# Performance work log

Hardware: AMD Instinct MI355X
Metric: run time of the kernel (lower is better)

## Reference

```python
import jax, jax.numpy as jnp
import numpy as np

B, M, T, N = 128, 256, 512, 512

def setup_inputs() -> dict:
    key = jax.random.key(0)
    ks = jax.random.split(key, 6)
    return {
        "hidden_state": jax.random.normal(ks[0], (B, M), jnp.float32),
        "cell_state": jax.random.normal(ks[1], (B, M), jnp.float32),
        "X": jax.random.normal(ks[2], (B, T, N), jnp.float32),
        "We1": jax.random.normal(ks[3], (2 * M, T), jnp.float32) * 0.05,
        "be1": jnp.zeros((T,), jnp.float32),
        "We2": jax.random.normal(ks[4], (T, T), jnp.float32) * 0.05,
        "be2": jnp.zeros((T,), jnp.float32),
        "v": jax.random.normal(ks[5], (T, 1), jnp.float32) * 0.05,
        "bv": jnp.zeros((1,), jnp.float32),
    }

def reference(hidden_state, cell_state, X, We1, be1, We2, be2, v, bv):
    # concat hidden + cell: [B, 2m]; Dense(T) then broadcast over n (K.repeat)
    hc = jnp.concatenate([hidden_state, cell_state], axis=-1)
    hs = (hc @ We1 + be1)[:, None, :]                 # [B, 1, T] (broadcast over n)
    # Permute X -> [B, n, T], Dense(T): contract over T
    ux = jnp.einsum('btn,tk->bnk', X, We2) + be2      # [B, n, T]
    # add + tanh + Dense(1) fused chain
    e = jnp.tanh(hs + ux) @ v + bv                    # [B, n, 1]
    # Permute -> [B, 1, n], softmax over last axis (n)
    attn = jax.nn.softmax(jnp.swapaxes(e, 1, 2), axis=-1)  # [B, 1, n]
    return attn
```

## Files before the change

### kernel.cpp

```cpp
#include <hip/hip_runtime.h>
#include <hip/hip_bf16.h>


typedef _Float16 half8 __attribute__((ext_vector_type(8)));
typedef _Float16 half2v __attribute__((ext_vector_type(2)));
typedef float floatx4 __attribute__((ext_vector_type(4)));

#define GLOAD_LDS16(gp, lp) __builtin_amdgcn_global_load_lds(                  \
    (const __attribute__((address_space(1))) void*)(const void*)(gp),          \
    (__attribute__((address_space(3))) void*)(void*)(lp), 16, 0, 0)

__device__ __forceinline__ float fast_tanh(float x) {
    float cx = fminf(15.0f, fmaxf(-15.0f, x));
    float e = __expf(2.0f * cx);
    return (e - 1.0f) * __fdividef(1.0f, e + 1.0f);
}

__global__ __launch_bounds__(256) void k_prep_a(const float* __restrict__ We2,
                                                _Float16* __restrict__ Af) {
    __shared__ float w2[32][512];
    const int ts = blockIdx.x;
    for (int idx = threadIdx.x; idx < 32 * 512; idx += 256) {
        int tl = idx >> 9, k = idx & 511;
        w2[tl][k] = We2[(ts * 32 + tl) * 512 + k];
    }
    __syncthreads();
    for (int item = threadIdx.x; item < 32 * 64; item += 256) {
        int c = item >> 6, l = item & 63;
        int k  = c * 16 + (l & 15);
        int tl = (l >> 4) * 8;
        half8 h;
#pragma unroll
        for (int j = 0; j < 8; ++j) h[j] = (_Float16)w2[tl + j][k];
        *(half8*)&Af[(((size_t)ts * 32 + c) * 64 + l) * 8] = h;
    }
}

__global__ __launch_bounds__(256) void k_hs(const float* __restrict__ hidden,
                                            const float* __restrict__ cell,
                                            const float* __restrict__ We1,
                                            const float* __restrict__ be1,
                                            const float* __restrict__ be2,
                                            float* __restrict__ g) {
    __shared__ __align__(16) float hcl[8][512];
    __shared__ float red[4][8][64];
    const int b0 = (blockIdx.x >> 3) << 3;
    const int k0 = (blockIdx.x & 7) << 6;
    for (int idx = threadIdx.x; idx < 8 * 512; idx += 256) {
        int bi = idx >> 9, j = idx & 511;
        hcl[bi][j] = (j < 256) ? hidden[(b0 + bi) * 256 + j]
                               : cell[(b0 + bi) * 256 + j - 256];
    }
    __syncthreads();
    const int kl = threadIdx.x & 63;
    const int jc = threadIdx.x >> 6;
    const int k  = k0 + kl;
    float acc[8] = {};
    for (int j = jc * 128; j < jc * 128 + 128; j += 4) {
        float w0 = We1[(j + 0) * 512 + k];
        float w1 = We1[(j + 1) * 512 + k];
        float w2 = We1[(j + 2) * 512 + k];
        float w3 = We1[(j + 3) * 512 + k];
#pragma unroll
        for (int bi = 0; bi < 8; ++bi) {
            float4 h = *(const float4*)&hcl[bi][j];
            acc[bi] += h.x * w0 + h.y * w1 + h.z * w2 + h.w * w3;
        }
    }
#pragma unroll
    for (int bi = 0; bi < 8; ++bi) red[jc][bi][kl] = acc[bi];
    __syncthreads();
    for (int idx = threadIdx.x; idx < 512; idx += 256) {
        int bi = idx >> 6, kk = idx & 63;
        float s = red[0][bi][kk] + red[1][bi][kk] + red[2][bi][kk] + red[3][bi][kk];
        int kg = k0 + kk;
        g[(b0 + bi) * 512 + kg] = s + be1[kg] + be2[kg];
    }
}

__global__ __launch_bounds__(256, 3) void k_main(const float* __restrict__ X,
                                                 const _Float16* __restrict__ Af,
                                                 const float* __restrict__ g,
                                                 const float* __restrict__ vvec,
                                                 float* __restrict__ Ep) {
    __shared__ __align__(16) float Xs[3][4096];
    const int tid  = threadIdx.x;
    const int lane = tid & 63;
    const int wv   = tid >> 6;
    const int l16  = lane & 15;
    const int lhi  = lane >> 4;
    const int logical = ((blockIdx.x & 7) << 8) | (blockIdx.x >> 3);
    const int kblk = logical & 1;
    const int nt   = (logical >> 1) & 7;
    const int b    = logical >> 4;
    const int n0   = nt << 6;

    const float* Xg = X + (size_t)b * 262144 + n0;
    const _Float16* AgW = Af + (size_t)(kblk * 16 + wv * 4) * 512 + (size_t)lane * 8;

    int xsrc[4], xdst[4];
#pragma unroll
    for (int p = 0; p < 4; ++p) {
        int t_loc = (wv << 4) + (p << 2) + (lane >> 4);
        int c_g   = (lane & 15) ^ (((t_loc >> 3) & 3) << 1);
        xsrc[p] = t_loc * 512 + c_g * 4;
        xdst[p] = ((wv << 4) + (p << 2)) * 64 + lane * 4;
    }
#define XDMA(s_, b_)                                                           \
    { _Pragma("unroll")                                                        \
      for (int p = 0; p < 4; ++p)                                              \
          GLOAD_LDS16(Xg + (size_t)(s_) * 32768 + xsrc[p], &Xs[b_][xdst[p]]); }

    const int q = l16 >> 2, r = l16 & 3;
    int boff[4];
#pragma unroll
    for (int nf = 0; nf < 4; ++nf)
        boff[nf] = lhi * 512 + ((((nf << 2) + q) ^ (lhi << 1)) << 2) + r;

    XDMA(0, 0);
    XDMA(1, 1);

    floatx4 acc[4][4];
#pragma unroll
    for (int a = 0; a < 4; ++a)
#pragma unroll
        for (int c = 0; c < 4; ++c) acc[a][c] = (floatx4){0.f, 0.f, 0.f, 0.f};

#pragma unroll
    for (int s = 0; s < 8; ++s) {
        const int buf = s % 3;
        if (s < 7) asm volatile("s_waitcnt vmcnt(4)" ::: "memory");
        else       asm volatile("s_waitcnt vmcnt(0)" ::: "memory");
        asm volatile("s_waitcnt lgkmcnt(0)" ::: "memory");
        __builtin_amdgcn_sched_barrier(0);
        __builtin_amdgcn_s_barrier();
        __builtin_amdgcn_sched_barrier(0);
        if (s + 2 < 8) XDMA(s + 2, (s + 2) % 3);
#pragma unroll
        for (int ko = 0; ko < 2; ++ko) {
            half8 af[4];
#pragma unroll
            for (int kf = 0; kf < 4; ++kf)
                af[kf] = *(const half8*)
                    (AgW + (size_t)(2 * s + ko) * 16384 + kf * 512);
            half8 bf[4];
#pragma unroll
            for (int nf = 0; nf < 4; ++nf) {
                union { half2v h2[4]; half8 h8; } u;
#pragma unroll
                for (int m = 0; m < 4; ++m) {
                    float f0 = Xs[buf][boff[nf] + ko * 2048 + (2 * m) * 64];
                    float f1 = Xs[buf][boff[nf] + ko * 2048 + (2 * m + 1) * 64];
                    u.h2[m] = __builtin_bit_cast(half2v,
                                  __builtin_amdgcn_cvt_pkrtz(f0, f1));
                }
                bf[nf] = u.h8;
            }
            __builtin_amdgcn_s_setprio(1);
#pragma unroll
            for (int kf = 0; kf < 4; ++kf)
#pragma unroll
                for (int nf = 0; nf < 4; ++nf)
                    acc[kf][nf] = __builtin_amdgcn_mfma_f32_16x16x32_f16(
                        af[kf], bf[nf], acc[kf][nf], 0, 0, 0);
            __builtin_amdgcn_s_setprio(0);
        }
    }
#undef XDMA

    const float* gb = g + b * 512;
    float sacc[4] = {0.f, 0.f, 0.f, 0.f};
#pragma unroll
    for (int kf = 0; kf < 4; ++kf) {
        const int kb = kblk * 256 + wv * 64 + kf * 16 + lhi * 4;
        float g0 = gb[kb + 0], g1 = gb[kb + 1], g2 = gb[kb + 2], g3 = gb[kb + 3];
        float v0 = vvec[kb + 0], v1 = vvec[kb + 1], v2 = vvec[kb + 2], v3 = vvec[kb + 3];
#pragma unroll
        for (int nf = 0; nf < 4; ++nf) {
            sacc[nf] += fast_tanh(acc[kf][nf][0] + g0) * v0;
            sacc[nf] += fast_tanh(acc[kf][nf][1] + g1) * v1;
            sacc[nf] += fast_tanh(acc[kf][nf][2] + g2) * v2;
            sacc[nf] += fast_tanh(acc[kf][nf][3] + g3) * v3;
        }
    }
#pragma unroll
    for (int nf = 0; nf < 4; ++nf) {
        sacc[nf] += __shfl_xor(sacc[nf], 16);
        sacc[nf] += __shfl_xor(sacc[nf], 32);
    }
    __syncthreads();
    float* ered = (float*)&Xs[0][0];
    if (lane < 16) {
#pragma unroll
        for (int nf = 0; nf < 4; ++nf) ered[wv * 64 + nf * 16 + l16] = sacc[nf];
    }
    __syncthreads();
    if (tid < 64) {
        float e = ered[tid] + ered[64 + tid] + ered[128 + tid] + ered[192 + tid];
        Ep[(size_t)kblk * 65536 + b * 512 + n0 + tid] = e;
    }
}

__global__ __launch_bounds__(256) void k_softmax(const float* __restrict__ Ep,
                                                 float* __restrict__ out) {
    __shared__ float rmax[4], rsum[4];
    const int b = blockIdx.x;
    const int tid = threadIdx.x;
    const float* E0 = Ep;
    const float* E1 = Ep + 65536;
    float e0 = E0[b * 512 + tid] + E1[b * 512 + tid];
    float e1 = E0[b * 512 + 256 + tid] + E1[b * 512 + 256 + tid];
    float m = fmaxf(e0, e1);
    for (int o = 32; o > 0; o >>= 1) m = fmaxf(m, __shfl_xor(m, o));
    if ((tid & 63) == 0) rmax[tid >> 6] = m;
    __syncthreads();
    m = fmaxf(fmaxf(rmax[0], rmax[1]), fmaxf(rmax[2], rmax[3]));
    float p0 = __expf(e0 - m), p1 = __expf(e1 - m);
    float ss = p0 + p1;
    for (int o = 32; o > 0; o >>= 1) ss += __shfl_xor(ss, o);
    if ((tid & 63) == 0) rsum[tid >> 6] = ss;
    __syncthreads();
    ss = rsum[0] + rsum[1] + rsum[2] + rsum[3];
    float inv = __fdividef(1.0f, ss);
    out[b * 512 + tid] = p0 * inv;
    out[b * 512 + 256 + tid] = p1 * inv;
}

extern "C" void kernel_launch(void* const* d_in, const int* in_sizes, int n_in,
                              void* d_out, int out_size, void* d_ws, size_t ws_size,
                              hipStream_t stream) {
    const float* hidden = (const float*)d_in[0];
    const float* cell   = (const float*)d_in[1];
    const float* X      = (const float*)d_in[2];
    const float* We1    = (const float*)d_in[3];
    const float* be1    = (const float*)d_in[4];
    const float* We2    = (const float*)d_in[5];
    const float* be2    = (const float*)d_in[6];
    const float* v      = (const float*)d_in[7];
    float* out = (float*)d_out;

    char* ws = (char*)d_ws;
    _Float16* Af = (_Float16*)ws;
    float* g     = (float*)(ws + 524288);
    float* Ep    = (float*)(ws + 786432);

    k_prep_a<<<16, 256, 0, stream>>>(We2, Af);
    k_hs<<<128, 256, 0, stream>>>(hidden, cell, We1, be1, be2, g);
    k_main<<<2048, 256, 0, stream>>>(X, Af, g, v, Ep);
    k_softmax<<<128, 256, 0, stream>>>(Ep, out);
}
```

Before: 83.23 us.

## Stage A fragments in LDS and split warps over k and n

```diff
diff --git a/kernel.cpp b/kernel.cpp
--- a/kernel.cpp
+++ b/kernel.cpp
@@ -78,125 +78,137 @@
     }
 }
 
-__global__ __launch_bounds__(256, 3) void k_main(const float* __restrict__ X,
+__global__ __launch_bounds__(256, 4) void k_main(const float* __restrict__ X,
                                                  const _Float16* __restrict__ Af,
                                                  const float* __restrict__ g,
                                                  const float* __restrict__ vvec,
                                                  float* __restrict__ Ep) {
-    __shared__ __align__(16) float Xs[3][4096];
+    __shared__ __align__(16) _Float16 Ab[8192];
+    __shared__ __align__(16) float    Xs[3][2048];
     const int tid  = threadIdx.x;
     const int lane = tid & 63;
     const int wv   = tid >> 6;
     const int l16  = lane & 15;
     const int lhi  = lane >> 4;
-    const int logical = ((blockIdx.x & 7) << 8) | (blockIdx.x >> 3);
+    const int kw   = wv & 1;
+    const int nw   = wv >> 1;
+    const int logical = (blockIdx.x & 7) * 256 + (blockIdx.x >> 3);
     const int kblk = logical & 1;
     const int nt   = (logical >> 1) & 7;
     const int b    = logical >> 4;
     const int n0   = nt << 6;
 
     const float* Xg = X + (size_t)b * 262144 + n0;
-    const _Float16* AgW = Af + (size_t)(kblk * 16 + wv * 4) * 512 + (size_t)lane * 8;
-
-    int xsrc[4], xdst[4];
-#pragma unroll
-    for (int p = 0; p < 4; ++p) {
-        int t_loc = (wv << 4) + (p << 2) + (lane >> 4);
+    const _Float16* Ag = Af + (size_t)(kblk * 16 + wv * 4) * 512 + (size_t)lane * 8;
+
+    int xsrc[2], xdst[2];
+#pragma unroll
+    for (int p = 0; p < 2; ++p) {
+        int t_loc = wv * 8 + p * 4 + (lane >> 4);
         int c_g   = (lane & 15) ^ (((t_loc >> 3) & 3) << 1);
         xsrc[p] = t_loc * 512 + c_g * 4;
-        xdst[p] = ((wv << 4) + (p << 2)) * 64 + lane * 4;
+        xdst[p] = (wv * 8 + p * 4) * 64 + lane * 4;
     }
 #define XDMA(s_, b_)                                                           \
     { _Pragma("unroll")                                                        \
-      for (int p = 0; p < 4; ++p)                                              \
-          GLOAD_LDS16(Xg + (size_t)(s_) * 32768 + xsrc[p], &Xs[b_][xdst[p]]); }
+      for (int p = 0; p < 2; ++p)                                              \
+          GLOAD_LDS16(Xg + (size_t)(s_) * 16384 + xsrc[p], &Xs[b_][xdst[p]]); }
+#define ADMA(s_)                                                               \
+    { _Pragma("unroll")                                                        \
+      for (int i = 0; i < 4; ++i)                                              \
+          GLOAD_LDS16(Ag + (size_t)(s_) * 16384 + i * 512,                     \
+                      &Ab[(wv * 4 + i) * 512 + lane * 8]); }
 
     const int q = l16 >> 2, r = l16 & 3;
-    int boff[4];
-#pragma unroll
-    for (int nf = 0; nf < 4; ++nf)
-        boff[nf] = lhi * 512 + ((((nf << 2) + q) ^ (lhi << 1)) << 2) + r;
+    int boff[2];
+#pragma unroll
+    for (int nf = 0; nf < 2; ++nf) {
+        int nfe = nw * 2 + nf;
+        boff[nf] = lhi * 512 + ((((nfe << 2) + q) ^ (lhi << 1)) << 2) + r;
+    }
 
     XDMA(0, 0);
+    ADMA(0);
     XDMA(1, 1);
 
-    floatx4 acc[4][4];
-#pragma unroll
-    for (int a = 0; a < 4; ++a)
-#pragma unroll
-        for (int c = 0; c < 4; ++c) acc[a][c] = (floatx4){0.f, 0.f, 0.f, 0.f};
-
-#pragma unroll
-    for (int s = 0; s < 8; ++s) {
+    floatx4 acc[8][2];
+#pragma unroll
+    for (int a = 0; a < 8; ++a) {
+        acc[a][0] = (floatx4){0.f, 0.f, 0.f, 0.f};
+        acc[a][1] = (floatx4){0.f, 0.f, 0.f, 0.f};
+    }
+
+#pragma unroll
+    for (int s = 0; s < 16; ++s) {
         const int buf = s % 3;
-        if (s < 7) asm volatile("s_waitcnt vmcnt(4)" ::: "memory");
-        else       asm volatile("s_waitcnt vmcnt(0)" ::: "memory");
+        if (s < 15) asm volatile("s_waitcnt vmcnt(2)" ::: "memory");
+        else        asm volatile("s_waitcnt vmcnt(0)" ::: "memory");
+        __builtin_amdgcn_sched_barrier(0);
+        __builtin_amdgcn_s_barrier();
+        __builtin_amdgcn_sched_barrier(0);
+        half8 af[8];
+#pragma unroll
+        for (int kf = 0; kf < 8; ++kf)
+            af[kf] = *(const half8*)&Ab[(kw * 8 + kf) * 512 + lane * 8];
+        half8 bf[2];
+#pragma unroll
+        for (int nf = 0; nf < 2; ++nf) {
+            union { half2v h2[4]; half8 h8; } u;
+#pragma unroll
+            for (int m = 0; m < 4; ++m) {
+                float f0 = Xs[buf][boff[nf] + (2 * m) * 64];
+                float f1 = Xs[buf][boff[nf] + (2 * m + 1) * 64];
+                u.h2[m] = __builtin_bit_cast(half2v,
+                              __builtin_amdgcn_cvt_pkrtz(f0, f1));
+            }
+            bf[nf] = u.h8;
+        }
         asm volatile("s_waitcnt lgkmcnt(0)" ::: "memory");
         __builtin_amdgcn_sched_barrier(0);
         __builtin_amdgcn_s_barrier();
         __builtin_amdgcn_sched_barrier(0);
-        if (s + 2 < 8) XDMA(s + 2, (s + 2) % 3);
-#pragma unroll
-        for (int ko = 0; ko < 2; ++ko) {
-            half8 af[4];
-#pragma unroll
-            for (int kf = 0; kf < 4; ++kf)
-                af[kf] = *(const half8*)
-                    (AgW + (size_t)(2 * s + ko) * 16384 + kf * 512);
-            half8 bf[4];
-#pragma unroll
-            for (int nf = 0; nf < 4; ++nf) {
-                union { half2v h2[4]; half8 h8; } u;
-#pragma unroll
-                for (int m = 0; m < 4; ++m) {
-                    float f0 = Xs[buf][boff[nf] + ko * 2048 + (2 * m) * 64];
-                    float f1 = Xs[buf][boff[nf] + ko * 2048 + (2 * m + 1) * 64];
-                    u.h2[m] = __builtin_bit_cast(half2v,
-                                  __builtin_amdgcn_cvt_pkrtz(f0, f1));
-                }
-                bf[nf] = u.h8;
-            }
-            __builtin_amdgcn_s_setprio(1);
-#pragma unroll
-            for (int kf = 0; kf < 4; ++kf)
-#pragma unroll
-                for (int nf = 0; nf < 4; ++nf)
-                    acc[kf][nf] = __builtin_amdgcn_mfma_f32_16x16x32_f16(
-                        af[kf], bf[nf], acc[kf][nf], 0, 0, 0);
-            __builtin_amdgcn_s_setprio(0);
+        if (s < 15) ADMA(s + 1);
+        if (s < 14) XDMA(s + 2, (s + 2) % 3);
+        __builtin_amdgcn_sched_barrier(0);
+        __builtin_amdgcn_s_setprio(1);
+#pragma unroll
+        for (int kf = 0; kf < 8; ++kf) {
+            acc[kf][0] = __builtin_amdgcn_mfma_f32_16x16x32_f16(af[kf], bf[0], acc[kf][0], 0, 0, 0);
+            acc[kf][1] = __builtin_amdgcn_mfma_f32_16x16x32_f16(af[kf], bf[1], acc[kf][1], 0, 0, 0);
         }
+        __builtin_amdgcn_s_setprio(0);
     }
 #undef XDMA
+#undef ADMA
 
     const float* gb = g + b * 512;
-    float sacc[4] = {0.f, 0.f, 0.f, 0.f};
-#pragma unroll
-    for (int kf = 0; kf < 4; ++kf) {
-        const int kb = kblk * 256 + wv * 64 + kf * 16 + lhi * 4;
+    float s0 = 0.f, s1 = 0.f;
+#pragma unroll
+    for (int kf = 0; kf < 8; ++kf) {
+        const int kb = kblk * 256 + kw * 128 + kf * 16 + lhi * 4;
         float g0 = gb[kb + 0], g1 = gb[kb + 1], g2 = gb[kb + 2], g3 = gb[kb + 3];
         float v0 = vvec[kb + 0], v1 = vvec[kb + 1], v2 = vvec[kb + 2], v3 = vvec[kb + 3];
-#pragma unroll
-        for (int nf = 0; nf < 4; ++nf) {
-            sacc[nf] += fast_tanh(acc[kf][nf][0] + g0) * v0;
-            sacc[nf] += fast_tanh(acc[kf][nf][1] + g1) * v1;
-            sacc[nf] += fast_tanh(acc[kf][nf][2] + g2) * v2;
-            sacc[nf] += fast_tanh(acc[kf][nf][3] + g3) * v3;
-        }
-    }
-#pragma unroll
-    for (int nf = 0; nf < 4; ++nf) {
-        sacc[nf] += __shfl_xor(sacc[nf], 16);
-        sacc[nf] += __shfl_xor(sacc[nf], 32);
-    }
-    __syncthreads();
-    float* ered = (float*)&Xs[0][0];
+        s0 += fast_tanh(acc[kf][0][0] + g0) * v0;
+        s0 += fast_tanh(acc[kf][0][1] + g1) * v1;
+        s0 += fast_tanh(acc[kf][0][2] + g2) * v2;
+        s0 += fast_tanh(acc[kf][0][3] + g3) * v3;
+        s1 += fast_tanh(acc[kf][1][0] + g0) * v0;
+        s1 += fast_tanh(acc[kf][1][1] + g1) * v1;
+        s1 += fast_tanh(acc[kf][1][2] + g2) * v2;
+        s1 += fast_tanh(acc[kf][1][3] + g3) * v3;
+    }
+    s0 += __shfl_xor(s0, 16);  s0 += __shfl_xor(s0, 32);
+    s1 += __shfl_xor(s1, 16);  s1 += __shfl_xor(s1, 32);
+
+    __syncthreads();
+    float* ered = (float*)&Ab[0];
     if (lane < 16) {
-#pragma unroll
-        for (int nf = 0; nf < 4; ++nf) ered[wv * 64 + nf * 16 + l16] = sacc[nf];
+        ered[kw * 64 + nw * 32 + 0  + l16] = s0;
+        ered[kw * 64 + nw * 32 + 16 + l16] = s1;
     }
     __syncthreads();
     if (tid < 64) {
-        float e = ered[tid] + ered[64 + tid] + ered[128 + tid] + ered[192 + tid];
+        float e = ered[tid] + ered[64 + tid];
         Ep[(size_t)kblk * 65536 + b * 512 + n0 + tid] = e;
     }
 }
```

New measurement: 80.95 us. 2.7% less time.

## Stage X through registers with fp16 conversion into a double-buffered LDS tile

Applied to the files above, without the earlier changes.

```diff
diff --git a/kernel.cpp b/kernel.cpp
--- a/kernel.cpp
+++ b/kernel.cpp
@@ -3,12 +3,7 @@
 
 
 typedef _Float16 half8 __attribute__((ext_vector_type(8)));
-typedef _Float16 half2v __attribute__((ext_vector_type(2)));
 typedef float floatx4 __attribute__((ext_vector_type(4)));
-
-#define GLOAD_LDS16(gp, lp) __builtin_amdgcn_global_load_lds(                  \
-    (const __attribute__((address_space(1))) void*)(const void*)(gp),          \
-    (__attribute__((address_space(3))) void*)(void*)(lp), 16, 0, 0)
 
 __device__ __forceinline__ float fast_tanh(float x) {
     float cx = fminf(15.0f, fmaxf(-15.0f, x));
@@ -83,42 +78,53 @@
                                                  const float* __restrict__ g,
                                                  const float* __restrict__ vvec,
                                                  float* __restrict__ Ep) {
-    __shared__ __align__(16) float Xs[3][4096];
+    __shared__ __align__(16) _Float16 Xb[2][2048];
     const int tid  = threadIdx.x;
     const int lane = tid & 63;
     const int wv   = tid >> 6;
     const int l16  = lane & 15;
     const int lhi  = lane >> 4;
-    const int logical = ((blockIdx.x & 7) << 8) | (blockIdx.x >> 3);
+    const int logical = (blockIdx.x & 7) * 256 + (blockIdx.x >> 3);
     const int kblk = logical & 1;
     const int nt   = (logical >> 1) & 7;
     const int b    = logical >> 4;
     const int n0   = nt << 6;
 
     const float* Xg = X + (size_t)b * 262144 + n0;
-    const _Float16* AgW = Af + (size_t)(kblk * 16 + wv * 4) * 512 + (size_t)lane * 8;
-
-    int xsrc[4], xdst[4];
-#pragma unroll
-    for (int p = 0; p < 4; ++p) {
-        int t_loc = (wv << 4) + (p << 2) + (lane >> 4);
-        int c_g   = (lane & 15) ^ (((t_loc >> 3) & 3) << 1);
-        xsrc[p] = t_loc * 512 + c_g * 4;
-        xdst[p] = ((wv << 4) + (p << 2)) * 64 + lane * 4;
-    }
-#define XDMA(s_, b_)                                                           \
-    { _Pragma("unroll")                                                        \
-      for (int p = 0; p < 4; ++p)                                              \
-          GLOAD_LDS16(Xg + (size_t)(s_) * 32768 + xsrc[p], &Xs[b_][xdst[p]]); }
-
-    const int q = l16 >> 2, r = l16 & 3;
-    int boff[4];
-#pragma unroll
-    for (int nf = 0; nf < 4; ++nf)
-        boff[nf] = lhi * 512 + ((((nf << 2) + q) ^ (lhi << 1)) << 2) + r;
-
-    XDMA(0, 0);
-    XDMA(1, 1);
+    const _Float16* Ag = Af + (size_t)(kblk * 16 + wv * 4) * 512 + (size_t)lane * 8;
+
+    const int xn = tid & 63;
+    const int xo = tid >> 6;
+    const float* Xt = Xg + (size_t)(xo * 8) * 512 + xn;
+    const int wslot = xn * 32 + ((xo ^ (xn & 3) ^ ((xn >> 2) & 3)) << 3);
+    int roff[4];
+#pragma unroll
+    for (int nf = 0; nf < 4; ++nf) {
+        int n = nf * 16 + l16;
+        roff[nf] = n * 32 + ((lhi ^ (n & 3) ^ ((n >> 2) & 3)) << 3);
+    }
+
+    float xs0[8], xs1[8], xs2[8];
+#define XLOAD(s_, arr_)                                                        \
+    do { _Pragma("unroll")                                                     \
+         for (int j = 0; j < 8; ++j)                                           \
+             arr_[j] = Xt[(size_t)(s_) * 16384 + (size_t)j * 512];             \
+    } while (0)
+#define XSTORE(s_, arr_)                                                       \
+    do { half8 h;                                                              \
+         _Pragma("unroll")                                                     \
+         for (int j = 0; j < 8; ++j) h[j] = (_Float16)arr_[j];                 \
+         *(half8*)&Xb[(s_) & 1][wslot] = h;                                    \
+    } while (0)
+
+    XLOAD(0, xs0);
+    XLOAD(1, xs1);
+    XLOAD(2, xs2);
+    XSTORE(0, xs0);
+    asm volatile("s_waitcnt lgkmcnt(0)" ::: "memory");
+    __builtin_amdgcn_sched_barrier(0);
+    __builtin_amdgcn_s_barrier();
+    __builtin_amdgcn_sched_barrier(0);
 
     floatx4 acc[4][4];
 #pragma unroll
@@ -127,46 +133,41 @@
         for (int c = 0; c < 4; ++c) acc[a][c] = (floatx4){0.f, 0.f, 0.f, 0.f};
 
 #pragma unroll
-    for (int s = 0; s < 8; ++s) {
-        const int buf = s % 3;
-        if (s < 7) asm volatile("s_waitcnt vmcnt(4)" ::: "memory");
-        else       asm volatile("s_waitcnt vmcnt(0)" ::: "memory");
+    for (int s = 0; s < 16; ++s) {
+        const int cur = s & 1;
+        half8 af[4];
+#pragma unroll
+        for (int kf = 0; kf < 4; ++kf)
+            af[kf] = *(const half8*)(Ag + (size_t)s * 16384 + (size_t)kf * 512);
+        if (s + 3 < 16) {
+            if ((s % 3) == 0)      XLOAD(s + 3, xs0);
+            else if ((s % 3) == 1) XLOAD(s + 3, xs1);
+            else                   XLOAD(s + 3, xs2);
+        }
+        half8 bf[4];
+#pragma unroll
+        for (int nf = 0; nf < 4; ++nf)
+            bf[nf] = *(const half8*)&Xb[cur][roff[nf]];
+        if (s + 1 < 16) {
+            if (((s + 1) % 3) == 0)      XSTORE(s + 1, xs0);
+            else if (((s + 1) % 3) == 1) XSTORE(s + 1, xs1);
+            else                         XSTORE(s + 1, xs2);
+        }
+        __builtin_amdgcn_s_setprio(1);
+#pragma unroll
+        for (int kf = 0; kf < 4; ++kf)
+#pragma unroll
+            for (int nf = 0; nf < 4; ++nf)
+                acc[kf][nf] = __builtin_amdgcn_mfma_f32_16x16x32_f16(
+                    af[kf], bf[nf], acc[kf][nf], 0, 0, 0);
+        __builtin_amdgcn_s_setprio(0);
         asm volatile("s_waitcnt lgkmcnt(0)" ::: "memory");
         __builtin_amdgcn_sched_barrier(0);
         __builtin_amdgcn_s_barrier();
         __builtin_amdgcn_sched_barrier(0);
-        if (s + 2 < 8) XDMA(s + 2, (s + 2) % 3);
-#pragma unroll
-        for (int ko = 0; ko < 2; ++ko) {
-            half8 af[4];
-#pragma unroll
-            for (int kf = 0; kf < 4; ++kf)
-                af[kf] = *(const half8*)
-                    (AgW + (size_t)(2 * s + ko) * 16384 + kf * 512);
-            half8 bf[4];
-#pragma unroll
-            for (int nf = 0; nf < 4; ++nf) {
-                union { half2v h2[4]; half8 h8; } u;
-#pragma unroll
-                for (int m = 0; m < 4; ++m) {
-                    float f0 = Xs[buf][boff[nf] + ko * 2048 + (2 * m) * 64];
-                    float f1 = Xs[buf][boff[nf] + ko * 2048 + (2 * m + 1) * 64];
-                    u.h2[m] = __builtin_bit_cast(half2v,
-                                  __builtin_amdgcn_cvt_pkrtz(f0, f1));
-                }
-                bf[nf] = u.h8;
-            }
-            __builtin_amdgcn_s_setprio(1);
-#pragma unroll
-            for (int kf = 0; kf < 4; ++kf)
-#pragma unroll
-                for (int nf = 0; nf < 4; ++nf)
-                    acc[kf][nf] = __builtin_amdgcn_mfma_f32_16x16x32_f16(
-                        af[kf], bf[nf], acc[kf][nf], 0, 0, 0);
-            __builtin_amdgcn_s_setprio(0);
-        }
-    }
-#undef XDMA
+    }
+#undef XLOAD
+#undef XSTORE
 
     const float* gb = g + b * 512;
     float sacc[4] = {0.f, 0.f, 0.f, 0.f};
@@ -189,7 +190,7 @@
         sacc[nf] += __shfl_xor(sacc[nf], 32);
     }
     __syncthreads();
-    float* ered = (float*)&Xs[0][0];
+    float* ered = (float*)&Xb[0][0];
     if (lane < 16) {
 #pragma unroll
         for (int nf = 0; nf < 4; ++nf) ered[wv * 64 + nf * 16 + l16] = sacc[nf];
```

New measurement: 78.42 us. 1.06x faster.

## Replace LDS triple-buffered X staging with direct per-lane global loads

Applied to the files above, without the earlier changes.

```diff
diff --git a/kernel.cpp b/kernel.cpp
--- a/kernel.cpp
+++ b/kernel.cpp
@@ -5,10 +5,6 @@
 typedef _Float16 half8 __attribute__((ext_vector_type(8)));
 typedef _Float16 half2v __attribute__((ext_vector_type(2)));
 typedef float floatx4 __attribute__((ext_vector_type(4)));
-
-#define GLOAD_LDS16(gp, lp) __builtin_amdgcn_global_load_lds(                  \
-    (const __attribute__((address_space(1))) void*)(const void*)(gp),          \
-    (__attribute__((address_space(3))) void*)(void*)(lp), 16, 0, 0)
 
 __device__ __forceinline__ float fast_tanh(float x) {
     float cx = fminf(15.0f, fmaxf(-15.0f, x));
@@ -83,42 +79,20 @@
                                                  const float* __restrict__ g,
                                                  const float* __restrict__ vvec,
                                                  float* __restrict__ Ep) {
-    __shared__ __align__(16) float Xs[3][4096];
+    __shared__ float ered[256];
     const int tid  = threadIdx.x;
     const int lane = tid & 63;
     const int wv   = tid >> 6;
     const int l16  = lane & 15;
     const int lhi  = lane >> 4;
-    const int logical = ((blockIdx.x & 7) << 8) | (blockIdx.x >> 3);
+    const int logical = (blockIdx.x & 7) * 256 + (blockIdx.x >> 3);
     const int kblk = logical & 1;
     const int nt   = (logical >> 1) & 7;
     const int b    = logical >> 4;
     const int n0   = nt << 6;
 
-    const float* Xg = X + (size_t)b * 262144 + n0;
-    const _Float16* AgW = Af + (size_t)(kblk * 16 + wv * 4) * 512 + (size_t)lane * 8;
-
-    int xsrc[4], xdst[4];
-#pragma unroll
-    for (int p = 0; p < 4; ++p) {
-        int t_loc = (wv << 4) + (p << 2) + (lane >> 4);
-        int c_g   = (lane & 15) ^ (((t_loc >> 3) & 3) << 1);
-        xsrc[p] = t_loc * 512 + c_g * 4;
-        xdst[p] = ((wv << 4) + (p << 2)) * 64 + lane * 4;
-    }
-#define XDMA(s_, b_)                                                           \
-    { _Pragma("unroll")                                                        \
-      for (int p = 0; p < 4; ++p)                                              \
-          GLOAD_LDS16(Xg + (size_t)(s_) * 32768 + xsrc[p], &Xs[b_][xdst[p]]); }
-
-    const int q = l16 >> 2, r = l16 & 3;
-    int boff[4];
-#pragma unroll
-    for (int nf = 0; nf < 4; ++nf)
-        boff[nf] = lhi * 512 + ((((nf << 2) + q) ^ (lhi << 1)) << 2) + r;
-
-    XDMA(0, 0);
-    XDMA(1, 1);
+    const float* Xb0 = X + (size_t)b * 262144 + (size_t)(lhi * 8) * 512 + n0 + l16;
+    const _Float16* Ag = Af + (size_t)(kblk * 16 + wv * 4) * 512 + (size_t)lane * 8;
 
     floatx4 acc[4][4];
 #pragma unroll
@@ -127,46 +101,32 @@
         for (int c = 0; c < 4; ++c) acc[a][c] = (floatx4){0.f, 0.f, 0.f, 0.f};
 
 #pragma unroll
-    for (int s = 0; s < 8; ++s) {
-        const int buf = s % 3;
-        if (s < 7) asm volatile("s_waitcnt vmcnt(4)" ::: "memory");
-        else       asm volatile("s_waitcnt vmcnt(0)" ::: "memory");
-        asm volatile("s_waitcnt lgkmcnt(0)" ::: "memory");
-        __builtin_amdgcn_sched_barrier(0);
-        __builtin_amdgcn_s_barrier();
-        __builtin_amdgcn_sched_barrier(0);
-        if (s + 2 < 8) XDMA(s + 2, (s + 2) % 3);
-#pragma unroll
-        for (int ko = 0; ko < 2; ++ko) {
-            half8 af[4];
-#pragma unroll
-            for (int kf = 0; kf < 4; ++kf)
-                af[kf] = *(const half8*)
-                    (AgW + (size_t)(2 * s + ko) * 16384 + kf * 512);
-            half8 bf[4];
-#pragma unroll
-            for (int nf = 0; nf < 4; ++nf) {
-                union { half2v h2[4]; half8 h8; } u;
-#pragma unroll
-                for (int m = 0; m < 4; ++m) {
-                    float f0 = Xs[buf][boff[nf] + ko * 2048 + (2 * m) * 64];
-                    float f1 = Xs[buf][boff[nf] + ko * 2048 + (2 * m + 1) * 64];
-                    u.h2[m] = __builtin_bit_cast(half2v,
-                                  __builtin_amdgcn_cvt_pkrtz(f0, f1));
-                }
-                bf[nf] = u.h8;
-            }
-            __builtin_amdgcn_s_setprio(1);
-#pragma unroll
-            for (int kf = 0; kf < 4; ++kf)
-#pragma unroll
-                for (int nf = 0; nf < 4; ++nf)
-                    acc[kf][nf] = __builtin_amdgcn_mfma_f32_16x16x32_f16(
-                        af[kf], bf[nf], acc[kf][nf], 0, 0, 0);
-            __builtin_amdgcn_s_setprio(0);
+    for (int s = 0; s < 16; ++s) {
+        half8 af[4];
+#pragma unroll
+        for (int kf = 0; kf < 4; ++kf)
+            af[kf] = *(const half8*)(Ag + (size_t)s * 16384 + (size_t)kf * 512);
+        half8 bf[4];
+#pragma unroll
+        for (int nf = 0; nf < 4; ++nf) {
+            float f[8];
+#pragma unroll
+            for (int j = 0; j < 8; ++j)
+                f[j] = Xb0[(size_t)(s * 32 + j) * 512 + nf * 16];
+            union { half2v h2[4]; half8 h8; } u;
+#pragma unroll
+            for (int m = 0; m < 4; ++m)
+                u.h2[m] = __builtin_bit_cast(half2v,
+                              __builtin_amdgcn_cvt_pkrtz(f[2 * m], f[2 * m + 1]));
+            bf[nf] = u.h8;
         }
-    }
-#undef XDMA
+#pragma unroll
+        for (int kf = 0; kf < 4; ++kf)
+#pragma unroll
+            for (int nf = 0; nf < 4; ++nf)
+                acc[kf][nf] = __builtin_amdgcn_mfma_f32_16x16x32_f16(
+                    af[kf], bf[nf], acc[kf][nf], 0, 0, 0);
+    }
 
     const float* gb = g + b * 512;
     float sacc[4] = {0.f, 0.f, 0.f, 0.f};
@@ -188,8 +148,6 @@
         sacc[nf] += __shfl_xor(sacc[nf], 16);
         sacc[nf] += __shfl_xor(sacc[nf], 32);
     }
-    __syncthreads();
-    float* ered = (float*)&Xs[0][0];
     if (lane < 16) {
 #pragma unroll
         for (int nf = 0; nf < 4; ++nf) ered[wv * 64 + nf * 16 + l16] = sacc[nf];
```

Result: slower. 87.11 us (+4.7%).
